# Kernel optimization log

Measured on AMD Instinct MI355X. Metric: run time of the kernel, lower is better.

## Reference

```python
import jax, jax.numpy as jnp
import numpy as np


def setup_inputs() -> dict:
    key = jax.random.key(0)
    ip = jax.random.normal(key, (8, 256, 128, 128), dtype=jnp.float32)
    return {"ip": ip}


def reference(ip):
    b, C, H, W = ip.shape
    two_c = 2 * C
    # precomputed complex shift grid: exp(-1j*2*pi*(C-0.5)*v/(2C)), v = 0..2C-1
    v = jnp.arange(two_c, dtype=jnp.float32)
    angle = -2.0 * jnp.pi * (C - 0.5) * v / two_c
    shift = (jnp.cos(angle) + 1j * jnp.sin(angle)).astype(jnp.complex64)  # [2C]

    viDct = ip * two_c                                   # [b, C, H, W]
    flip_neg = -viDct[:, 1:][:, ::-1]                    # [b, C-1, H, W]
    zeros = jnp.zeros((b, 1, H, W), dtype=ip.dtype)
    rev = jnp.concatenate([viDct, zeros, flip_neg], axis=1)  # [b, 2C, H, W]
    rev = rev.astype(jnp.complex64) * shift[None, :, None, None]
    vxx = jnp.fft.ifft(rev, axis=1)                      # norm='backward' (default)
    out = vxx[:, :C][:, ::-1].real                       # first C, flipped, real part
    return out.astype(ip.dtype)
```

## Files before the change

### kernel.cpp

```cpp
#include <hip/hip_runtime.h>
#include <math.h>

#define NB   8
#define NC   256
#define NHW  (128 * 128)


#define BK 64
#define NITER (NC / BK)
#define ABUF 16384
#define XLDS 32768
#define XBUF 4096

typedef __attribute__((ext_vector_type(4))) float f32x4;
typedef __attribute__((ext_vector_type(8))) short bf16x8;
typedef __attribute__((ext_vector_type(4))) unsigned int u32x4;

__device__ __forceinline__ unsigned short f2bf(float f) {
    unsigned u = __builtin_bit_cast(unsigned, f);
    u += 0x7fffu + ((u >> 16) & 1u);
    return (unsigned short)(u >> 16);
}

__device__ __forceinline__ unsigned pack2bf(float a, float b) {
    unsigned lo = __builtin_bit_cast(unsigned, a);
    lo += 0x7fffu + ((lo >> 16) & 1u);
    unsigned hi = __builtin_bit_cast(unsigned, b);
    hi += 0x7fffu + ((hi >> 16) & 1u);
    return (lo >> 16) | (hi & 0xffff0000u);
}

__device__ __forceinline__ bf16x8 flip_odd(bf16x8 b) {
    u32x4 u = __builtin_bit_cast(u32x4, b);
    u ^= (u32x4){0x80000000u, 0x80000000u, 0x80000000u, 0x80000000u};
    return __builtin_bit_cast(bf16x8, u);
}

__global__ void coef_kernel(unsigned short* __restrict__ coef) {
    int idx = blockIdx.x * 256 + threadIdx.x;
    int c = idx >> 8;
    int k = idx & 255;
    int t = (k * (2 * c + 1)) & 1023;
    float v = (k == 0) ? 1.0f : 2.0f * cosf((float)t * (float)(M_PI / 512.0));
    coef[idx] = f2bf(v);
}

__device__ __forceinline__ void gload_lds16(const void* g, void* l) {
    __builtin_amdgcn_global_load_lds(
        (const __attribute__((address_space(1))) unsigned int*)g,
        (__attribute__((address_space(3))) unsigned int*)l,
        16, 0, 0);
}


__global__ __launch_bounds__(256, 4)
void dct_gemm(const float* __restrict__ X, const unsigned short* __restrict__ Mcoef,
              float* __restrict__ Out) {
    __shared__ __align__(16) unsigned char lds[40960];

    const int tid  = threadIdx.x;
    const int lane = tid & 63;
    const int wave = tid >> 6;
    const int m16  = lane & 15;
    const int quad = lane >> 4;

    const int p0 = blockIdx.x * 32;
    const size_t base = (size_t)blockIdx.y * (NC * NHW);
    const float* Xg = X + base;
    float* Ob = Out + base + p0;

    const int aRowT = tid >> 3;
    const int aSlot = (tid & 7) ^ (aRowT & 7);
    const unsigned short* aS = Mcoef + aRowT * NC + aSlot * 8;
    const int aDst = tid * 16;

    const int sp = tid & 31;
    const int g  = tid >> 5;
    const float* xS = Xg + (size_t)(g * 8) * NHW + p0 + sp;
    const int xWoff = sp * 128 + (((g ^ (sp & 7)) & 7) << 4);

    f32x4 acc[2][2][2];
#pragma unroll
    for (int a = 0; a < 2; a++)
#pragma unroll
        for (int b = 0; b < 2; b++)
#pragma unroll
            for (int h = 0; h < 2; h++) acc[a][b][h] = (f32x4){0.f, 0.f, 0.f, 0.f};

    {
        float v[8];
#pragma unroll
        for (int j = 0; j < 8; j++) v[j] = xS[(size_t)j * NHW];
#pragma unroll
        for (int i = 0; i < 4; i++)
            gload_lds16(aS + i * 32 * NC, lds + i * 4096 + aDst);
        int4 q = { (int)pack2bf(v[0], v[1]), (int)pack2bf(v[2], v[3]),
                   (int)pack2bf(v[4], v[5]), (int)pack2bf(v[6], v[7]) };
        *(int4*)(lds + XLDS + xWoff) = q;
    }
    __syncthreads();

    const int aB = (wave * 32 + m16) * 128;
    const int xB = m16 * 128;
    const int rs = m16 & 7;

    for (int t = 0; t < NITER; t++) {
        const int cb = t & 1;
        const unsigned char* Ac = lds + cb * ABUF;
        const unsigned char* Xc = lds + XLDS + cb * XBUF;

        float v[8];
        if (t + 1 < NITER) {
            const int k1 = (t + 1) * BK;
#pragma unroll
            for (int j = 0; j < 8; j++) v[j] = xS[(size_t)(k1 + j) * NHW];
#pragma unroll
            for (int i = 0; i < 4; i++)
                gload_lds16(aS + i * 32 * NC + k1, lds + (cb ^ 1) * ABUF + i * 4096 + aDst);
        }

#pragma unroll
        for (int kk = 0; kk < 2; kk++) {
            const int so = (((kk * 4 + quad) ^ rs) << 4);
            bf16x8 af0 = *(const bf16x8*)(Ac + aB + so);
            bf16x8 af1 = *(const bf16x8*)(Ac + aB + 16 * 128 + so);
            bf16x8 bf0 = *(const bf16x8*)(Xc + xB + so);
            bf16x8 bf1 = *(const bf16x8*)(Xc + xB + 16 * 128 + so);
            bf16x8 bn0 = flip_odd(bf0);
            bf16x8 bn1 = flip_odd(bf1);
            acc[0][0][0] = __builtin_amdgcn_mfma_f32_16x16x32_bf16(af0, bf0, acc[0][0][0], 0, 0, 0);
            acc[0][1][0] = __builtin_amdgcn_mfma_f32_16x16x32_bf16(af0, bf1, acc[0][1][0], 0, 0, 0);
            acc[1][0][0] = __builtin_amdgcn_mfma_f32_16x16x32_bf16(af1, bf0, acc[1][0][0], 0, 0, 0);
            acc[1][1][0] = __builtin_amdgcn_mfma_f32_16x16x32_bf16(af1, bf1, acc[1][1][0], 0, 0, 0);
            acc[0][0][1] = __builtin_amdgcn_mfma_f32_16x16x32_bf16(af0, bn0, acc[0][0][1], 0, 0, 0);
            acc[0][1][1] = __builtin_amdgcn_mfma_f32_16x16x32_bf16(af0, bn1, acc[0][1][1], 0, 0, 0);
            acc[1][0][1] = __builtin_amdgcn_mfma_f32_16x16x32_bf16(af1, bn0, acc[1][0][1], 0, 0, 0);
            acc[1][1][1] = __builtin_amdgcn_mfma_f32_16x16x32_bf16(af1, bn1, acc[1][1][1], 0, 0, 0);
        }

        if (t + 1 < NITER) {
            int4 q = { (int)pack2bf(v[0], v[1]), (int)pack2bf(v[2], v[3]),
                       (int)pack2bf(v[4], v[5]), (int)pack2bf(v[6], v[7]) };
            *(int4*)(lds + XLDS + (cb ^ 1) * XBUF + xWoff) = q;
            __syncthreads();
        }
    }

#pragma unroll
    for (int mt = 0; mt < 2; mt++) {
        const int cS = wave * 32 + mt * 16 + quad * 4;
#pragma unroll
        for (int nt = 0; nt < 2; nt++) {
            float* o = Ob + nt * 16 + m16;
#pragma unroll
            for (int r = 0; r < 4; r++) {
                o[(size_t)(cS + r) * NHW]       = acc[mt][nt][0][r];
                o[(size_t)(255 - cS - r) * NHW] = acc[mt][nt][1][r];
            }
        }
    }
}

extern "C" void kernel_launch(void* const* d_in, const int* in_sizes, int n_in,
                              void* d_out, int out_size, void* d_ws, size_t ws_size,
                              hipStream_t stream) {
    const float* ip = (const float*)d_in[0];
    float* out = (float*)d_out;
    unsigned short* coef = (unsigned short*)d_ws;

    coef_kernel<<<dim3(128), dim3(256), 0, stream>>>(coef);

    dct_gemm<<<dim3(NHW / 32, NB), dim3(256), 0, stream>>>(ip, coef, out);
}
```

Baseline: 242.7 us.

## Retile DCT GEMM to 64 pixels by 64 coefficients with swapped MFMA operands

Each block now computes 64 pixels by 64 coefficient pairs instead of 32 pixels by all 128 pairs, using a 2x2 wave arrangement and a 1D grid remapped so that consecutive blocks are spread across batches and coefficient halves. The MFMA operands are swapped so the accumulator rows run along pixels, which lets the epilogue write contiguous float4 stores instead of scalar stores. LDS use drops to 32 KB and the occupancy hint rises to 5 blocks. The trade-off is that each input pixel tile is now read from global memory twice, once per coefficient half, in exchange for wider stores and higher occupancy.

```diff
diff --git a/kernel.cpp b/kernel.cpp
--- a/kernel.cpp
+++ b/kernel.cpp
@@ -8,9 +8,9 @@
 
 #define BK 64
 #define NITER (NC / BK)
-#define ABUF 16384
-#define XLDS 32768
-#define XBUF 4096
+#define ABUF 8192
+#define XLDS 16384
+#define XBUF 8192
 
 typedef __attribute__((ext_vector_type(4))) float f32x4;
 typedef __attribute__((ext_vector_type(8))) short bf16x8;
@@ -53,55 +53,67 @@
 }
 
 
-__global__ __launch_bounds__(256, 4)
+__global__ __launch_bounds__(256, 5)
 void dct_gemm(const float* __restrict__ X, const unsigned short* __restrict__ Mcoef,
               float* __restrict__ Out) {
-    __shared__ __align__(16) unsigned char lds[40960];
+    __shared__ __align__(16) unsigned char lds[32768];
 
     const int tid  = threadIdx.x;
     const int lane = tid & 63;
     const int wave = tid >> 6;
     const int m16  = lane & 15;
     const int quad = lane >> 4;
+    const int pw   = wave & 1;
+    const int cw   = wave >> 1;
 
-    const int p0 = blockIdx.x * 32;
-    const size_t base = (size_t)blockIdx.y * (NC * NHW);
+    const int w  = (blockIdx.x & 7) * 512 + (blockIdx.x >> 3);
+    const int b  = w >> 9;
+    const int ct = (w >> 8) & 1;
+    const int pt = w & 255;
+
+    const int p0 = pt * 64;
+    const size_t base = (size_t)b * (NC * NHW);
     const float* Xg = X + base;
     float* Ob = Out + base + p0;
 
-    const int aRowT = tid >> 3;
-    const int aSlot = (tid & 7) ^ (aRowT & 7);
-    const unsigned short* aS = Mcoef + aRowT * NC + aSlot * 8;
+    const int aRow  = tid >> 3;
+    const int aSlot = (tid & 7) ^ (aRow & 7);
+    const unsigned short* aS = Mcoef + (ct * 64 + aRow) * NC + aSlot * 8;
     const int aDst = tid * 16;
 
-    const int sp = tid & 31;
-    const int g  = tid >> 5;
-    const float* xS = Xg + (size_t)(g * 8) * NHW + p0 + sp;
-    const int xWoff = sp * 128 + (((g ^ (sp & 7)) & 7) << 4);
+    const int sp = tid & 63;
+    const int kg = tid >> 6;
+    const float* xS = Xg + (size_t)(kg * 8) * NHW + p0 + sp;
+    const int xW0 = XLDS + sp * 128 + (((kg    ) ^ (sp & 7)) << 4);
+    const int xW1 = XLDS + sp * 128 + (((kg + 4) ^ (sp & 7)) << 4);
 
     f32x4 acc[2][2][2];
 #pragma unroll
-    for (int a = 0; a < 2; a++)
+    for (int i = 0; i < 2; i++)
 #pragma unroll
-        for (int b = 0; b < 2; b++)
+        for (int j = 0; j < 2; j++)
 #pragma unroll
-            for (int h = 0; h < 2; h++) acc[a][b][h] = (f32x4){0.f, 0.f, 0.f, 0.f};
+            for (int h = 0; h < 2; h++) acc[i][j][h] = (f32x4){0.f, 0.f, 0.f, 0.f};
 
     {
-        float v[8];
+        float v[16];
 #pragma unroll
-        for (int j = 0; j < 8; j++) v[j] = xS[(size_t)j * NHW];
+        for (int j = 0; j < 8; j++) v[j]     = xS[(size_t)j * NHW];
 #pragma unroll
-        for (int i = 0; i < 4; i++)
-            gload_lds16(aS + i * 32 * NC, lds + i * 4096 + aDst);
-        int4 q = { (int)pack2bf(v[0], v[1]), (int)pack2bf(v[2], v[3]),
-                   (int)pack2bf(v[4], v[5]), (int)pack2bf(v[6], v[7]) };
-        *(int4*)(lds + XLDS + xWoff) = q;
+        for (int j = 0; j < 8; j++) v[8 + j] = xS[(size_t)(32 + j) * NHW];
+        gload_lds16(aS, lds + aDst);
+        gload_lds16(aS + 32 * NC, lds + 4096 + aDst);
+        int4 q0 = { (int)pack2bf(v[0], v[1]),  (int)pack2bf(v[2], v[3]),
+                    (int)pack2bf(v[4], v[5]),  (int)pack2bf(v[6], v[7]) };
+        int4 q1 = { (int)pack2bf(v[8], v[9]),  (int)pack2bf(v[10], v[11]),
+                    (int)pack2bf(v[12], v[13]), (int)pack2bf(v[14], v[15]) };
+        *(int4*)(lds + xW0) = q0;
+        *(int4*)(lds + xW1) = q1;
     }
     __syncthreads();
 
-    const int aB = (wave * 32 + m16) * 128;
-    const int xB = m16 * 128;
+    const int aB = (cw * 32 + m16) * 128;
+    const int xB = (pw * 32 + m16) * 128;
     const int rs = m16 & 7;
 
     for (int t = 0; t < NITER; t++) {
@@ -109,54 +121,55 @@
         const unsigned char* Ac = lds + cb * ABUF;
         const unsigned char* Xc = lds + XLDS + cb * XBUF;
 
-        float v[8];
+        float v[16];
         if (t + 1 < NITER) {
             const int k1 = (t + 1) * BK;
 #pragma unroll
-            for (int j = 0; j < 8; j++) v[j] = xS[(size_t)(k1 + j) * NHW];
+            for (int j = 0; j < 8; j++) v[j]     = xS[(size_t)(k1 + j) * NHW];
 #pragma unroll
-            for (int i = 0; i < 4; i++)
-                gload_lds16(aS + i * 32 * NC + k1, lds + (cb ^ 1) * ABUF + i * 4096 + aDst);
+            for (int j = 0; j < 8; j++) v[8 + j] = xS[(size_t)(k1 + 32 + j) * NHW];
+            gload_lds16(aS + k1, lds + (cb ^ 1) * ABUF + aDst);
+            gload_lds16(aS + 32 * NC + k1, lds + (cb ^ 1) * ABUF + 4096 + aDst);
         }
 
 #pragma unroll
         for (int kk = 0; kk < 2; kk++) {
             const int so = (((kk * 4 + quad) ^ rs) << 4);
-            bf16x8 af0 = *(const bf16x8*)(Ac + aB + so);
-            bf16x8 af1 = *(const bf16x8*)(Ac + aB + 16 * 128 + so);
-            bf16x8 bf0 = *(const bf16x8*)(Xc + xB + so);
-            bf16x8 bf1 = *(const bf16x8*)(Xc + xB + 16 * 128 + so);
-            bf16x8 bn0 = flip_odd(bf0);
-            bf16x8 bn1 = flip_odd(bf1);
-            acc[0][0][0] = __builtin_amdgcn_mfma_f32_16x16x32_bf16(af0, bf0, acc[0][0][0], 0, 0, 0);
-            acc[0][1][0] = __builtin_amdgcn_mfma_f32_16x16x32_bf16(af0, bf1, acc[0][1][0], 0, 0, 0);
-            acc[1][0][0] = __builtin_amdgcn_mfma_f32_16x16x32_bf16(af1, bf0, acc[1][0][0], 0, 0, 0);
-            acc[1][1][0] = __builtin_amdgcn_mfma_f32_16x16x32_bf16(af1, bf1, acc[1][1][0], 0, 0, 0);
-            acc[0][0][1] = __builtin_amdgcn_mfma_f32_16x16x32_bf16(af0, bn0, acc[0][0][1], 0, 0, 0);
-            acc[0][1][1] = __builtin_amdgcn_mfma_f32_16x16x32_bf16(af0, bn1, acc[0][1][1], 0, 0, 0);
-            acc[1][0][1] = __builtin_amdgcn_mfma_f32_16x16x32_bf16(af1, bn0, acc[1][0][1], 0, 0, 0);
-            acc[1][1][1] = __builtin_amdgcn_mfma_f32_16x16x32_bf16(af1, bn1, acc[1][1][1], 0, 0, 0);
+            bf16x8 xf0 = *(const bf16x8*)(Xc + xB + so);
+            bf16x8 xf1 = *(const bf16x8*)(Xc + xB + 2048 + so);
+            bf16x8 mf0 = *(const bf16x8*)(Ac + aB + so);
+            bf16x8 mf1 = *(const bf16x8*)(Ac + aB + 2048 + so);
+            bf16x8 mn0 = flip_odd(mf0);
+            bf16x8 mn1 = flip_odd(mf1);
+            acc[0][0][0] = __builtin_amdgcn_mfma_f32_16x16x32_bf16(xf0, mf0, acc[0][0][0], 0, 0, 0);
+            acc[0][1][0] = __builtin_amdgcn_mfma_f32_16x16x32_bf16(xf0, mf1, acc[0][1][0], 0, 0, 0);
+            acc[1][0][0] = __builtin_amdgcn_mfma_f32_16x16x32_bf16(xf1, mf0, acc[1][0][0], 0, 0, 0);
+            acc[1][1][0] = __builtin_amdgcn_mfma_f32_16x16x32_bf16(xf1, mf1, acc[1][1][0], 0, 0, 0);
+            acc[0][0][1] = __builtin_amdgcn_mfma_f32_16x16x32_bf16(xf0, mn0, acc[0][0][1], 0, 0, 0);
+            acc[0][1][1] = __builtin_amdgcn_mfma_f32_16x16x32_bf16(xf0, mn1, acc[0][1][1], 0, 0, 0);
+            acc[1][0][1] = __builtin_amdgcn_mfma_f32_16x16x32_bf16(xf1, mn0, acc[1][0][1], 0, 0, 0);
+            acc[1][1][1] = __builtin_amdgcn_mfma_f32_16x16x32_bf16(xf1, mn1, acc[1][1][1], 0, 0, 0);
         }
 
         if (t + 1 < NITER) {
-            int4 q = { (int)pack2bf(v[0], v[1]), (int)pack2bf(v[2], v[3]),
-                       (int)pack2bf(v[4], v[5]), (int)pack2bf(v[6], v[7]) };
-            *(int4*)(lds + XLDS + (cb ^ 1) * XBUF + xWoff) = q;
+            int4 q0 = { (int)pack2bf(v[0], v[1]),  (int)pack2bf(v[2], v[3]),
+                        (int)pack2bf(v[4], v[5]),  (int)pack2bf(v[6], v[7]) };
+            int4 q1 = { (int)pack2bf(v[8], v[9]),  (int)pack2bf(v[10], v[11]),
+                        (int)pack2bf(v[12], v[13]), (int)pack2bf(v[14], v[15]) };
+            *(int4*)(lds + (cb ^ 1) * XBUF + xW0) = q0;
+            *(int4*)(lds + (cb ^ 1) * XBUF + xW1) = q1;
             __syncthreads();
         }
     }
 
 #pragma unroll
-    for (int mt = 0; mt < 2; mt++) {
-        const int cS = wave * 32 + mt * 16 + quad * 4;
+    for (int cn = 0; cn < 2; cn++) {
+        const int cLoc = ct * 64 + cw * 32 + cn * 16 + m16;
 #pragma unroll
-        for (int nt = 0; nt < 2; nt++) {
-            float* o = Ob + nt * 16 + m16;
-#pragma unroll
-            for (int r = 0; r < 4; r++) {
-                o[(size_t)(cS + r) * NHW]       = acc[mt][nt][0][r];
-                o[(size_t)(255 - cS - r) * NHW] = acc[mt][nt][1][r];
-            }
+        for (int pm = 0; pm < 2; pm++) {
+            const int pp = pw * 32 + pm * 16 + quad * 4;
+            *(f32x4*)(Ob + (size_t)cLoc * NHW + pp)         = acc[pm][cn][0];
+            *(f32x4*)(Ob + (size_t)(255 - cLoc) * NHW + pp) = acc[pm][cn][1];
         }
     }
 }
@@ -170,5 +183,5 @@
 
     coef_kernel<<<dim3(128), dim3(256), 0, stream>>>(coef);
 
-    dct_gemm<<<dim3(NHW / 32, NB), dim3(256), 0, stream>>>(ip, coef, out);
+    dct_gemm<<<dim3(4096), dim3(256), 0, stream>>>(ip, coef, out);
 }
```

Measured after the change: 258.7 us. 1.07x slower.
